# Kernel optimization log

Hardware: AMD Instinct MI355X
Metric: run time of the kernel (lower is better)

Reference implementation:

```python
import jax, jax.numpy as jnp
import numpy as np

N = 100000          # nodes
E = 1_600_000       # edges (before self loops)
F_IN = 128          # node features
H = 4               # heads (gat1)
C = 32              # dim_h
HC = H * C
NC_CLONE = 20 - 1
NC_TYPE = 30 - 1
NEG_SLOPE = 0.2
BN_EPS = 1e-5


def setup_inputs() -> dict:
    key = jax.random.key(0)
    ks = jax.random.split(key, 24)
    rn = lambda k, shape, s=0.1: (jax.random.normal(k, shape, jnp.float32) * s)
    inp = {
        "x": jax.random.normal(ks[0], (N, F_IN), jnp.float32),
        "edge_index": jax.random.randint(ks[1], (2, E), 0, N, jnp.int32),
        "edge_attr": jax.random.uniform(ks[2], (E, 1), jnp.float32),
        # gat1 (GATv2Conv F_IN -> C, heads=H, edge_dim=1)
        "Wl1": rn(ks[3], (F_IN, HC)), "Wr1": rn(ks[4], (F_IN, HC)),
        "We1": rn(ks[5], (1, HC)), "att1": rn(ks[6], (H, C)), "b1": rn(ks[7], (HC,)),
        # skip Linear F_IN -> HC
        "skip_W": rn(ks[8], (F_IN, HC)), "skip_b": rn(ks[9], (HC,)),
        # batchnorm1
        "bn_g": jnp.ones((HC,), jnp.float32), "bn_b": jnp.zeros((HC,), jnp.float32),
        # gat2 (GATv2Conv HC -> C, heads=1, edge_dim=1)
        "Wl2": rn(ks[10], (HC, C)), "Wr2": rn(ks[11], (HC, C)),
        "We2": rn(ks[12], (1, C)), "att2": rn(ks[13], (1, C)), "b2": rn(ks[14], (C,)),
        # heads
        "fc1_W": rn(ks[15], (C, C)), "fc1_b": rn(ks[16], (C,)),
        "Wc": rn(ks[17], (C, NC_CLONE)), "bc": rn(ks[18], (NC_CLONE,)),
        "Wt": rn(ks[19], (C, NC_TYPE)), "bt": rn(ks[20], (NC_TYPE,)),
    }
    return inp


def _add_self_loops(src, dst, eattr, n):
    # PyG add_self_loops with fill_value='mean': loop attr = scatter-mean of edge_attr by dst
    deg = jax.ops.segment_sum(jnp.ones_like(eattr[:, 0]), dst, num_segments=n)
    mean_attr = jax.ops.segment_sum(eattr, dst, num_segments=n) / jnp.clip(deg, 1.0)[:, None]
    loop = jnp.arange(n, dtype=src.dtype)
    return (jnp.concatenate([src, loop]), jnp.concatenate([dst, loop]),
            jnp.concatenate([eattr, mean_attr], axis=0))


def _gatv2(x, src, dst, eattr, Wl, Wr, We, att, bias, heads, ch):
    n = x.shape[0]
    xl = (x @ Wl).reshape(n, heads, ch)   # values & source attention feats
    xr = (x @ Wr).reshape(n, heads, ch)   # target attention feats
    ee = (eattr @ We).reshape(-1, heads, ch)
    m = jax.nn.leaky_relu(xl[src] + xr[dst] + ee, NEG_SLOPE)   # [E,H,C]
    alpha = jnp.einsum('ehc,hc->eh', m, att)                   # [E,H]
    amax = jax.ops.segment_max(alpha, dst, num_segments=n)
    amax = jnp.where(jnp.isfinite(amax), amax, 0.0)
    ex = jnp.exp(alpha - amax[dst])
    den = jax.ops.segment_sum(ex, dst, num_segments=n)
    a = ex / (den[dst] + 1e-16)                                # segment softmax
    out = jax.ops.segment_sum(a[..., None] * xl[src], dst, num_segments=n)
    return out.reshape(n, heads * ch) + bias, a


def reference(x, edge_index, edge_attr, Wl1, Wr1, We1, att1, b1, skip_W, skip_b,
              bn_g, bn_b, Wl2, Wr2, We2, att2, b2, fc1_W, fc1_b, Wc, bc, Wt, bt):
    n = x.shape[0]
    src, dst, ea = _add_self_loops(edge_index[0], edge_index[1], edge_attr, n)
    h, _ = _gatv2(x, src, dst, ea, Wl1, Wr1, We1, att1, b1, H, C)
    h = h + x @ skip_W + skip_b
    mu = jnp.mean(h, axis=0)
    var = jnp.mean(jnp.square(h - mu), axis=0)
    h = (h - mu) * jax.lax.rsqrt(var + BN_EPS) * bn_g + bn_b
    h = jax.nn.elu(h)
    h, w = _gatv2(h, src, dst, ea, Wl2, Wr2, We2, att2, b2, 1, C)
    h = jax.nn.elu(h)
    h_last = jax.nn.relu(h @ fc1_W + fc1_b)
    h_type = jax.nn.log_softmax(h_last @ Wt + bt, axis=1)
    h_clone = jax.nn.log_softmax(h_last @ Wc + bc, axis=1)
    out = jnp.concatenate([h_clone, h_type], axis=1)
    return out, w
```

## Files before the change

kernel.cpp:

```cpp
#include <hip/hip_runtime.h>
#include <math.h>

#define NN 100000
#define EE 1600000
#define FIN 128
#define HCH 128
#define CCH 32
#define NCLONE 19
#define NTYPE 29
#define ETOT (EE + NN)
#define SCAN_B 49

typedef __bf16 bf16_t;
typedef bf16_t bf16x2 __attribute__((ext_vector_type(2)));
typedef bf16_t bf16x4 __attribute__((ext_vector_type(4)));
typedef bf16_t bf16x8 __attribute__((ext_vector_type(8)));
typedef float f32x4 __attribute__((ext_vector_type(4)));

__global__ __launch_bounds__(256) void k_wcvt(const float* __restrict__ Wl1,
                                              const float* __restrict__ Wr1,
                                              const float* __restrict__ Ws,
                                              const float* __restrict__ Wl2,
                                              const float* __restrict__ Wr2,
                                              bf16_t* __restrict__ WbT,
                                              bf16_t* __restrict__ Wb2T) {
    int t = blockIdx.x * 256 + threadIdx.x;
    if (t < 384 * 128) {
        int n = t >> 7, k = t & 127;
        const float* W = (n < 128) ? Wl1 : ((n < 256) ? Wr1 : Ws);
        WbT[t] = (bf16_t)W[k * 128 + (n & 127)];
    } else if (t < 384 * 128 + 64 * 128) {
        int u = t - 384 * 128;
        int n = u >> 7, k = u & 127;
        const float* W = (n < 32) ? Wl2 : Wr2;
        Wb2T[u] = (bf16_t)W[k * 32 + (n & 31)];
    }
}

__global__ __launch_bounds__(256) void k_deg(const int* __restrict__ ei,
                                             int* __restrict__ deg,
                                             int* __restrict__ slot) {
    int e = blockIdx.x * 256 + threadIdx.x;
    if (e < EE) {
        int d = ei[EE + e];
        slot[e] = atomicAdd(&deg[d], 1);
    }
}

__global__ __launch_bounds__(256) void k_scan1(const int* __restrict__ deg,
                                               int* __restrict__ offs,
                                               int* __restrict__ bsum) {
    __shared__ int tsum[256];
    int b = blockIdx.x, tid = threadIdx.x;
    int base = b * 2048;
    int loc[8];
    int s = 0;
    #pragma unroll
    for (int i = 0; i < 8; ++i) {
        int idx = base + tid * 8 + i;
        int d = (idx < NN) ? deg[idx] : 0;
        loc[i] = s; s += d;
    }
    tsum[tid] = s;
    __syncthreads();
    for (int off = 1; off < 256; off <<= 1) {
        int v = (tid >= off) ? tsum[tid - off] : 0;
        __syncthreads();
        tsum[tid] += v;
        __syncthreads();
    }
    int texcl = tsum[tid] - s;
    #pragma unroll
    for (int i = 0; i < 8; ++i) {
        int idx = base + tid * 8 + i;
        if (idx < NN) offs[idx] = texcl + loc[i];
    }
    if (tid == 255) bsum[b] = tsum[255];
}

__global__ void k_scan2(int* __restrict__ bsum) {
    if (threadIdx.x == 0) {
        int run = 0;
        for (int i = 0; i < SCAN_B; ++i) { int t = bsum[i]; bsum[i] = run; run += t; }
    }
}

__global__ __launch_bounds__(256) void k_scan3(int* __restrict__ offs,
                                               const int* __restrict__ bsum) {
    int i = blockIdx.x * 256 + threadIdx.x;
    if (i < NN) offs[i] += bsum[i >> 11];
}

__global__ __launch_bounds__(256) void k_fill(const int* __restrict__ ei,
                                              const float* __restrict__ ea,
                                              const int* __restrict__ offs,
                                              const int* __restrict__ slot,
                                              int2* __restrict__ ep8,
                                              int* __restrict__ eid) {
    int e = blockIdx.x * 256 + threadIdx.x;
    if (e < EE) {
        int d = ei[EE + e];
        int pos = offs[d] + slot[e];
        ep8[pos] = make_int2(ei[e], __float_as_int(ea[e]));
        eid[pos] = e;
    }
}

__global__ __launch_bounds__(256) void k_gemm1(const float* __restrict__ x,
                                               const bf16_t* __restrict__ WbT,
                                               bf16_t* __restrict__ xl,
                                               bf16_t* __restrict__ xr,
                                               bf16_t* __restrict__ sk) {
    __shared__ bf16_t As[128 * 128];
    __shared__ bf16_t Bs[128 * 128];
    const int tid = threadIdx.x;
    const int row0 = blockIdx.x * 128;
    const int chunk = blockIdx.y;
    const int col0 = chunk * 128;
    bf16_t* __restrict__ out = (chunk == 0) ? xl : ((chunk == 1) ? xr : sk);
    #pragma unroll
    for (int i = 0; i < 8; ++i) {
        int c = i * 256 + tid;
        int r = c >> 4, g = c & 15;
        int gr = row0 + r;
        bf16x8 v = {};
        if (gr < NN) {
            float4 f0 = *(const float4*)(x + (size_t)gr * 128 + g * 8);
            float4 f1 = *(const float4*)(x + (size_t)gr * 128 + g * 8 + 4);
            v[0] = (bf16_t)f0.x; v[1] = (bf16_t)f0.y; v[2] = (bf16_t)f0.z; v[3] = (bf16_t)f0.w;
            v[4] = (bf16_t)f1.x; v[5] = (bf16_t)f1.y; v[6] = (bf16_t)f1.z; v[7] = (bf16_t)f1.w;
        }
        *(bf16x8*)&As[r * 128 + ((g ^ (r & 7)) * 8)] = v;
    }
    #pragma unroll
    for (int i = 0; i < 8; ++i) {
        int c = i * 256 + tid;
        int n = c >> 4, g = c & 15;
        bf16x8 v = *(const bf16x8*)(WbT + (size_t)(col0 + n) * 128 + g * 8);
        *(bf16x8*)&Bs[n * 128 + ((g ^ (n & 7)) * 8)] = v;
    }
    __syncthreads();

    const int wid = tid >> 6, lane = tid & 63;
    const int wm = wid >> 1, wn = wid & 1;
    const int lr = lane & 15, lg = lane >> 4;
    f32x4 acc[4][4] = {};
    #pragma unroll
    for (int ks = 0; ks < 4; ++ks) {
        int g = ks * 4 + lg;
        bf16x8 b[4];
        #pragma unroll
        for (int ni = 0; ni < 4; ++ni) {
            int n = wn * 64 + ni * 16 + lr;
            b[ni] = *(const bf16x8*)&Bs[n * 128 + ((g ^ (n & 7)) * 8)];
        }
        #pragma unroll
        for (int mi = 0; mi < 4; ++mi) {
            int r = wm * 64 + mi * 16 + lr;
            bf16x8 a = *(const bf16x8*)&As[r * 128 + ((g ^ (r & 7)) * 8)];
            #pragma unroll
            for (int ni = 0; ni < 4; ++ni)
                acc[mi][ni] = __builtin_amdgcn_mfma_f32_16x16x32_bf16(a, b[ni], acc[mi][ni], 0, 0, 0);
        }
    }
    #pragma unroll
    for (int mi = 0; mi < 4; ++mi)
        #pragma unroll
        for (int ni = 0; ni < 4; ++ni)
            #pragma unroll
            for (int j = 0; j < 4; ++j) {
                int gr = row0 + wm * 64 + mi * 16 + lg * 4 + j;
                if (gr >= NN) continue;
                int n = wn * 64 + ni * 16 + lr;
                out[(size_t)gr * 128 + n] = (bf16_t)acc[mi][ni][j];
            }
}

__global__ __launch_bounds__(256) void k_gat1(const bf16_t* __restrict__ xl1,
                                              const bf16_t* __restrict__ xr1,
                                              const bf16_t* __restrict__ skb,
                                              const int* __restrict__ offs,
                                              const int* __restrict__ deg,
                                              const int2* __restrict__ ep8,
                                              const float* __restrict__ att1,
                                              const float* __restrict__ we1,
                                              const float* __restrict__ b1,
                                              const float* __restrict__ skipb,
                                              bf16_t* __restrict__ hb,
                                              float* __restrict__ mattr) {
    int v = (blockIdx.x * 256 + threadIdx.x) >> 6;
    if (v >= NN) return;
    int lane = threadIdx.x & 63;
    int sub = lane >> 4;
    int l = lane & 15;
    int c0 = l * 8;
    float at[8], we[8], xr[8];
    {
        float4 t0 = *(const float4*)(att1 + c0);
        float4 t1 = *(const float4*)(att1 + c0 + 4);
        at[0] = t0.x; at[1] = t0.y; at[2] = t0.z; at[3] = t0.w;
        at[4] = t1.x; at[5] = t1.y; at[6] = t1.z; at[7] = t1.w;
        float4 w0 = *(const float4*)(we1 + c0);
        float4 w1 = *(const float4*)(we1 + c0 + 4);
        we[0] = w0.x; we[1] = w0.y; we[2] = w0.z; we[3] = w0.w;
        we[4] = w1.x; we[5] = w1.y; we[6] = w1.z; we[7] = w1.w;
        bf16x8 xrv = *(const bf16x8*)(xr1 + (size_t)v * 128 + c0);
        #pragma unroll
        for (int j = 0; j < 8; ++j) xr[j] = (float)xrv[j];
    }
    float mr = -1e30f, den = 0.f, easum = 0.f;
    float n[8] = {};
    int st = offs[v], dg = deg[v];
    int i = sub;
    int2 e0 = make_int2(0, 0), e1 = make_int2(0, 0);
    bf16x8 a0 = {};
    if (i < dg) e0 = ep8[st + i];
    if (i + 4 < dg) e1 = ep8[st + i + 4];
    if (i < dg) a0 = *(const bf16x8*)(xl1 + (size_t)e0.x * 128 + c0);
    for (; i < dg; i += 4) {
        bf16x8 a1 = {};
        int2 e2 = make_int2(0, 0);
        if (i + 4 < dg) a1 = *(const bf16x8*)(xl1 + (size_t)e1.x * 128 + c0);
        if (i + 8 < dg) e2 = ep8[st + i + 8];
        float ea_ = __int_as_float(e0.y);
        easum += ea_;
        float q = 0.f, xv[8];
        #pragma unroll
        for (int j = 0; j < 8; ++j) {
            xv[j] = (float)a0[j];
            float w_ = xv[j] + fmaf(ea_, we[j], xr[j]);
            w_ = (w_ > 0.f) ? w_ : 0.2f * w_;
            q = fmaf(w_, at[j], q);
        }
        q += __shfl_xor(q, 1, 4);
        q += __shfl_xor(q, 2, 4);
        float nm = fmaxf(mr, q);
        float ex = __expf(q - nm);
        if (nm > mr) {
            float sc = __expf(mr - nm);
            den *= sc;
            #pragma unroll
            for (int j = 0; j < 8; ++j) n[j] *= sc;
            mr = nm;
        }
        den += ex;
        #pragma unroll
        for (int j = 0; j < 8; ++j) n[j] = fmaf(ex, xv[j], n[j]);
        e0 = e1; a0 = a1; e1 = e2;
    }
    #pragma unroll
    for (int w_ = 16; w_ <= 32; w_ <<= 1) {
        float mo = __shfl_xor(mr, w_, 64);
        float dn = __shfl_xor(den, w_, 64);
        float es = __shfl_xor(easum, w_, 64);
        float o[8];
        #pragma unroll
        for (int j = 0; j < 8; ++j) o[j] = __shfl_xor(n[j], w_, 64);
        float M = fmaxf(mr, mo);
        float sa = __expf(mr - M), sb = __expf(mo - M);
        den = den * sa + dn * sb;
        #pragma unroll
        for (int j = 0; j < 8; ++j) n[j] = n[j] * sa + o[j] * sb;
        mr = M;
        easum += es;
    }
    float eav = easum / fmaxf((float)dg, 1.0f);
    if (lane == 0) mattr[v] = eav;
    bf16x8 svv = *(const bf16x8*)(xl1 + (size_t)v * 128 + c0);
    float qs = 0.f, xs[8];
    #pragma unroll
    for (int j = 0; j < 8; ++j) {
        xs[j] = (float)svv[j];
        float w_ = xs[j] + fmaf(eav, we[j], xr[j]);
        w_ = (w_ > 0.f) ? w_ : 0.2f * w_;
        qs = fmaf(w_, at[j], qs);
    }
    qs += __shfl_xor(qs, 1, 4);
    qs += __shfl_xor(qs, 2, 4);
    {
        float nm = fmaxf(mr, qs);
        float ex = __expf(qs - nm);
        if (nm > mr) {
            float sc = __expf(mr - nm);
            den *= sc;
            #pragma unroll
            for (int j = 0; j < 8; ++j) n[j] *= sc;
            mr = nm;
        }
        den += ex;
        #pragma unroll
        for (int j = 0; j < 8; ++j) n[j] = fmaf(ex, xs[j], n[j]);
    }
    if (sub == 0) {
        float inv = 1.0f / (den + 1e-16f);
        float4 bb0 = *(const float4*)(b1 + c0);
        float4 bb1 = *(const float4*)(b1 + c0 + 4);
        float4 sb0 = *(const float4*)(skipb + c0);
        float4 sb1 = *(const float4*)(skipb + c0 + 4);
        bf16x8 skv = *(const bf16x8*)(skb + (size_t)v * 128 + c0);
        float bb[8] = {bb0.x, bb0.y, bb0.z, bb0.w, bb1.x, bb1.y, bb1.z, bb1.w};
        float sv[8] = {sb0.x, sb0.y, sb0.z, sb0.w, sb1.x, sb1.y, sb1.z, sb1.w};
        bf16x8 r;
        #pragma unroll
        for (int j = 0; j < 8; ++j)
            r[j] = (bf16_t)(n[j] * inv + bb[j] + (float)skv[j] + sv[j]);
        *(bf16x8*)(hb + (size_t)v * 128 + c0) = r;
    }
}

__global__ __launch_bounds__(256) void k_bnstats(const bf16_t* __restrict__ h,
                                                 float* __restrict__ bns,
                                                 float* __restrict__ bnq) {
    __shared__ float sS[16 * 128];
    __shared__ float sQ[16 * 128];
    int tid = threadIdx.x;
    int cg = tid & 15;
    int slot = tid >> 4;
    int c0 = cg * 8;
    float s[8] = {}, q[8] = {};
    for (int r = blockIdx.x * 16 + slot; r < NN; r += gridDim.x * 16) {
        bf16x8 v = *(const bf16x8*)&h[(size_t)r * 128 + c0];
        #pragma unroll
        for (int j = 0; j < 8; ++j) { float f = (float)v[j]; s[j] += f; q[j] += f * f; }
    }
    #pragma unroll
    for (int j = 0; j < 8; ++j) { sS[slot * 128 + c0 + j] = s[j]; sQ[slot * 128 + c0 + j] = q[j]; }
    __syncthreads();
    if (tid < 128) {
        float as = 0.f, aq = 0.f;
        #pragma unroll
        for (int k = 0; k < 16; ++k) { as += sS[k * 128 + tid]; aq += sQ[k * 128 + tid]; }
        atomicAdd(&bns[tid], as);
        atomicAdd(&bnq[tid], aq);
    }
}

__global__ void k_bnfinal(const float* __restrict__ bns, const float* __restrict__ bnq,
                          const float* __restrict__ g, const float* __restrict__ b,
                          float* __restrict__ scale, float* __restrict__ shift) {
    int c = threadIdx.x;
    if (c < 128) {
        float mu = bns[c] * (1.0f / NN);
        float var = bnq[c] * (1.0f / NN) - mu * mu;
        float rs = rsqrtf(var + 1e-5f);
        float a = rs * g[c];
        scale[c] = a;
        shift[c] = b[c] - mu * a;
    }
}

__global__ __launch_bounds__(256) void k_gemm2(const bf16_t* __restrict__ h,
                                               const float* __restrict__ scl,
                                               const float* __restrict__ shf,
                                               const bf16_t* __restrict__ Wb2T,
                                               bf16_t* __restrict__ xl2,
                                               float* __restrict__ xr2) {
    __shared__ bf16_t As[128 * 128];
    __shared__ bf16_t Bs[64 * 128];
    const int tid = threadIdx.x;
    const int row0 = blockIdx.x * 128;
    #pragma unroll
    for (int i = 0; i < 8; ++i) {
        int c = i * 256 + tid;
        int r = c >> 4, g = c & 15;
        int gr = row0 + r;
        bf16x8 v = {};
        if (gr < NN) {
            bf16x8 hv = *(const bf16x8*)(h + (size_t)gr * 128 + g * 8);
            float4 s0 = *(const float4*)(scl + g * 8);
            float4 s1 = *(const float4*)(scl + g * 8 + 4);
            float4 t0 = *(const float4*)(shf + g * 8);
            float4 t1 = *(const float4*)(shf + g * 8 + 4);
            float e[8];
            e[0] = (float)hv[0] * s0.x + t0.x; e[1] = (float)hv[1] * s0.y + t0.y;
            e[2] = (float)hv[2] * s0.z + t0.z; e[3] = (float)hv[3] * s0.w + t0.w;
            e[4] = (float)hv[4] * s1.x + t1.x; e[5] = (float)hv[5] * s1.y + t1.y;
            e[6] = (float)hv[6] * s1.z + t1.z; e[7] = (float)hv[7] * s1.w + t1.w;
            #pragma unroll
            for (int j = 0; j < 8; ++j) {
                float vv = e[j];
                vv = (vv > 0.f) ? vv : (__expf(vv) - 1.0f);
                v[j] = (bf16_t)vv;
            }
        }
        *(bf16x8*)&As[r * 128 + ((g ^ (r & 7)) * 8)] = v;
    }
    #pragma unroll
    for (int i = 0; i < 4; ++i) {
        int c = i * 256 + tid;
        int n = c >> 4, g = c & 15;
        bf16x8 v = *(const bf16x8*)(Wb2T + (size_t)n * 128 + g * 8);
        *(bf16x8*)&Bs[n * 128 + ((g ^ (n & 7)) * 8)] = v;
    }
    __syncthreads();

    const int wid = tid >> 6, lane = tid & 63;
    const int wm = wid >> 1, wn = wid & 1;
    const int lr = lane & 15, lg = lane >> 4;
    f32x4 acc[4][2] = {};
    #pragma unroll
    for (int ks = 0; ks < 4; ++ks) {
        int g = ks * 4 + lg;
        bf16x8 b0, b1;
        {
            int n = wn * 32 + lr;
            b0 = *(const bf16x8*)&Bs[n * 128 + ((g ^ (n & 7)) * 8)];
            n += 16;
            b1 = *(const bf16x8*)&Bs[n * 128 + ((g ^ (n & 7)) * 8)];
        }
        #pragma unroll
        for (int mi = 0; mi < 4; ++mi) {
            int r = wm * 64 + mi * 16 + lr;
            bf16x8 a = *(const bf16x8*)&As[r * 128 + ((g ^ (r & 7)) * 8)];
            acc[mi][0] = __builtin_amdgcn_mfma_f32_16x16x32_bf16(a, b0, acc[mi][0], 0, 0, 0);
            acc[mi][1] = __builtin_amdgcn_mfma_f32_16x16x32_bf16(a, b1, acc[mi][1], 0, 0, 0);
        }
    }
    #pragma unroll
    for (int mi = 0; mi < 4; ++mi)
        #pragma unroll
        for (int ni = 0; ni < 2; ++ni)
            #pragma unroll
            for (int j = 0; j < 4; ++j) {
                int gr = row0 + wm * 64 + mi * 16 + lg * 4 + j;
                if (gr >= NN) continue;
                int n = wn * 32 + ni * 16 + lr;
                float val = acc[mi][ni][j];
                if (n < 32) xl2[(size_t)gr * 32 + n] = (bf16_t)val;
                else xr2[(size_t)gr * 32 + (n - 32)] = val;
            }
}

__global__ __launch_bounds__(256) void k_gat2(const bf16_t* __restrict__ xl2,
                                              const float* __restrict__ xr2,
                                              const float* __restrict__ mattr,
                                              const int* __restrict__ offs,
                                              const int* __restrict__ deg,
                                              const int2* __restrict__ ep8,
                                              const int* __restrict__ eid,
                                              const float* __restrict__ att2,
                                              const float* __restrict__ we2,
                                              const float* __restrict__ b2,
                                              float* __restrict__ h3,
                                              float* __restrict__ wout) {
    int v = (blockIdx.x * 256 + threadIdx.x) >> 6;
    if (v >= NN) return;
    int lane = threadIdx.x & 63;
    int sub = lane >> 3;
    int l = lane & 7;
    int c0 = l * 4;
    float4 atv = *(const float4*)(att2 + c0);
    float4 wev = *(const float4*)(we2 + c0);
    float4 xrv = *(const float4*)(xr2 + (size_t)v * 32 + c0);
    float at[4] = {atv.x, atv.y, atv.z, atv.w};
    float we[4] = {wev.x, wev.y, wev.z, wev.w};
    float xr[4] = {xrv.x, xrv.y, xrv.z, xrv.w};
    float mr = -1e30f, den = 0.f;
    float n[4] = {};
    int st = offs[v], dg = deg[v];
    int i = sub;
    int2 e0 = make_int2(0, 0), e1 = make_int2(0, 0);
    bf16x4 a0 = {};
    if (i < dg) e0 = ep8[st + i];
    if (i + 8 < dg) e1 = ep8[st + i + 8];
    if (i < dg) a0 = *(const bf16x4*)(xl2 + (size_t)e0.x * 32 + c0);
    for (; i < dg; i += 8) {
        bf16x4 a1 = {};
        int2 e2 = make_int2(0, 0);
        if (i + 8 < dg) a1 = *(const bf16x4*)(xl2 + (size_t)e1.x * 32 + c0);
        if (i + 16 < dg) e2 = ep8[st + i + 16];
        int ide = eid[st + i];
        float ea_ = __int_as_float(e0.y);
        float q = 0.f, xv[4];
        #pragma unroll
        for (int j = 0; j < 4; ++j) {
            xv[j] = (float)a0[j];
            float w_ = xv[j] + fmaf(ea_, we[j], xr[j]);
            w_ = (w_ > 0.f) ? w_ : 0.2f * w_;
            q = fmaf(w_, at[j], q);
        }
        q += __shfl_xor(q, 1, 8);
        q += __shfl_xor(q, 2, 8);
        q += __shfl_xor(q, 4, 8);
        if (l == 0) wout[ide] = q;
        float nm = fmaxf(mr, q);
        float ex = __expf(q - nm);
        if (nm > mr) {
            float sc = __expf(mr - nm);
            den *= sc;
            #pragma unroll
            for (int j = 0; j < 4; ++j) n[j] *= sc;
            mr = nm;
        }
        den += ex;
        #pragma unroll
        for (int j = 0; j < 4; ++j) n[j] = fmaf(ex, xv[j], n[j]);
        e0 = e1; a0 = a1; e1 = e2;
    }
    #pragma unroll
    for (int w_ = 8; w_ <= 32; w_ <<= 1) {
        float mo = __shfl_xor(mr, w_, 64);
        float dn = __shfl_xor(den, w_, 64);
        float o[4];
        #pragma unroll
        for (int j = 0; j < 4; ++j) o[j] = __shfl_xor(n[j], w_, 64);
        float M = fmaxf(mr, mo);
        float sa = __expf(mr - M), sb = __expf(mo - M);
        den = den * sa + dn * sb;
        #pragma unroll
        for (int j = 0; j < 4; ++j) n[j] = n[j] * sa + o[j] * sb;
        mr = M;
    }
    float eav = mattr[v];
    bf16x4 sv = *(const bf16x4*)(xl2 + (size_t)v * 32 + c0);
    float qs = 0.f, xs[4];
    #pragma unroll
    for (int j = 0; j < 4; ++j) {
        xs[j] = (float)sv[j];
        float w_ = xs[j] + fmaf(eav, we[j], xr[j]);
        w_ = (w_ > 0.f) ? w_ : 0.2f * w_;
        qs = fmaf(w_, at[j], qs);
    }
    qs += __shfl_xor(qs, 1, 8);
    qs += __shfl_xor(qs, 2, 8);
    qs += __shfl_xor(qs, 4, 8);
    {
        float nm = fmaxf(mr, qs);
        float ex = __expf(qs - nm);
        if (nm > mr) {
            float sc = __expf(mr - nm);
            den *= sc;
            #pragma unroll
            for (int j = 0; j < 4; ++j) n[j] *= sc;
            mr = nm;
        }
        den += ex;
        #pragma unroll
        for (int j = 0; j < 4; ++j) n[j] = fmaf(ex, xs[j], n[j]);
    }
    float inv = 1.0f / (den + 1e-16f);
    if (lane == 0) wout[EE + v] = __expf(qs - mr) * inv;
    if (l == 0) {
        for (int k = sub; k < dg; k += 8) {
            int ide = eid[st + k];
            float q = wout[ide];
            wout[ide] = __expf(q - mr) * inv;
        }
    }
    if (sub == 0) {
        float4 bb = *(const float4*)(b2 + c0);
        float b_[4] = {bb.x, bb.y, bb.z, bb.w};
        float4 r;
        float* rp = &r.x;
        #pragma unroll
        for (int j = 0; j < 4; ++j) {
            float o = n[j] * inv + b_[j];
            rp[j] = (o > 0.f) ? o : (__expf(o) - 1.0f);
        }
        *(float4*)(h3 + (size_t)v * 32 + c0) = r;
    }
}

__global__ __launch_bounds__(256) void k_head(const float* __restrict__ h3,
                                              const float* __restrict__ fc1W,
                                              const float* __restrict__ fc1b,
                                              const float* __restrict__ Wc,
                                              const float* __restrict__ bc,
                                              const float* __restrict__ Wt,
                                              const float* __restrict__ bt,
                                              float* __restrict__ outp) {
    __shared__ float sW1[32 * 32];
    __shared__ float sWc[32 * NCLONE];
    __shared__ float sWt[32 * NTYPE];
    __shared__ float sb1[32], sbc[NCLONE], sbt[NTYPE];
    int tid = threadIdx.x;
    for (int i = tid; i < 1024; i += 256) sW1[i] = fc1W[i];
    for (int i = tid; i < 32 * NCLONE; i += 256) sWc[i] = Wc[i];
    for (int i = tid; i < 32 * NTYPE; i += 256) sWt[i] = Wt[i];
    if (tid < 32) sb1[tid] = fc1b[tid];
    if (tid < NCLONE) sbc[tid] = bc[tid];
    if (tid < NTYPE) sbt[tid] = bt[tid];
    __syncthreads();
    int g = tid >> 5, l = tid & 31;
    int v = blockIdx.x * 8 + g;
    if (v >= NN) return;
    float x = h3[(size_t)v * CCH + l];
    float acc = sb1[l];
    #pragma unroll
    for (int c = 0; c < 32; ++c) {
        float xc = __shfl(x, c, 32);
        acc += xc * sW1[c * 32 + l];
    }
    float hl = fmaxf(acc, 0.0f);
    float at = (l < NTYPE) ? sbt[l] : 0.0f;
    float ac = (l < NCLONE) ? sbc[l] : 0.0f;
    #pragma unroll
    for (int c = 0; c < 32; ++c) {
        float hc = __shfl(hl, c, 32);
        float wt_ = (l < NTYPE) ? sWt[c * NTYPE + l] : 0.0f;
        float wc_ = (l < NCLONE) ? sWc[c * NCLONE + l] : 0.0f;
        at += hc * wt_;
        ac += hc * wc_;
    }
    float vt = (l < NTYPE) ? at : -INFINITY;
    float mt = vt;
    mt = fmaxf(mt, __shfl_xor(mt, 16, 32));
    mt = fmaxf(mt, __shfl_xor(mt, 8, 32));
    mt = fmaxf(mt, __shfl_xor(mt, 4, 32));
    mt = fmaxf(mt, __shfl_xor(mt, 2, 32));
    mt = fmaxf(mt, __shfl_xor(mt, 1, 32));
    float et = __expf(vt - mt);
    float stt = et;
    stt += __shfl_xor(stt, 16, 32);
    stt += __shfl_xor(stt, 8, 32);
    stt += __shfl_xor(stt, 4, 32);
    stt += __shfl_xor(stt, 2, 32);
    stt += __shfl_xor(stt, 1, 32);
    float lt = vt - mt - logf(stt);
    float vc = (l < NCLONE) ? ac : -INFINITY;
    float mc = vc;
    mc = fmaxf(mc, __shfl_xor(mc, 16, 32));
    mc = fmaxf(mc, __shfl_xor(mc, 8, 32));
    mc = fmaxf(mc, __shfl_xor(mc, 4, 32));
    mc = fmaxf(mc, __shfl_xor(mc, 2, 32));
    mc = fmaxf(mc, __shfl_xor(mc, 1, 32));
    float ec = __expf(vc - mc);
    float sc = ec;
    sc += __shfl_xor(sc, 16, 32);
    sc += __shfl_xor(sc, 8, 32);
    sc += __shfl_xor(sc, 4, 32);
    sc += __shfl_xor(sc, 2, 32);
    sc += __shfl_xor(sc, 1, 32);
    float lc = vc - mc - logf(sc);
    size_t ob = (size_t)v * 48;
    if (l < NCLONE) outp[ob + l] = lc;
    if (l < NTYPE) outp[ob + NCLONE + l] = lt;
}

extern "C" void kernel_launch(void* const* d_in, const int* in_sizes, int n_in,
                              void* d_out, int out_size, void* d_ws, size_t ws_size,
                              hipStream_t stream) {
    const float* x     = (const float*)d_in[0];
    const int*   ei    = (const int*)d_in[1];
    const float* ea    = (const float*)d_in[2];
    const float* Wl1   = (const float*)d_in[3];
    const float* Wr1   = (const float*)d_in[4];
    const float* We1   = (const float*)d_in[5];
    const float* att1  = (const float*)d_in[6];
    const float* b1    = (const float*)d_in[7];
    const float* skipW = (const float*)d_in[8];
    const float* skipb = (const float*)d_in[9];
    const float* bng   = (const float*)d_in[10];
    const float* bnb   = (const float*)d_in[11];
    const float* Wl2   = (const float*)d_in[12];
    const float* Wr2   = (const float*)d_in[13];
    const float* We2   = (const float*)d_in[14];
    const float* att2  = (const float*)d_in[15];
    const float* b2    = (const float*)d_in[16];
    const float* fc1W  = (const float*)d_in[17];
    const float* fc1b  = (const float*)d_in[18];
    const float* Wc    = (const float*)d_in[19];
    const float* bc    = (const float*)d_in[20];
    const float* Wt    = (const float*)d_in[21];
    const float* bt    = (const float*)d_in[22];
    float* out = (float*)d_out;
    float* wout = out + (size_t)NN * 48;

    const size_t NF = (size_t)NN * FIN;
    char* w = (char*)d_ws;
    bf16_t* xl1b = (bf16_t*)w;  w += NF * 2;
    bf16_t* xr1b = (bf16_t*)w;  w += NF * 2;
    bf16_t* skb  = (bf16_t*)w;  w += NF * 2;
    bf16_t* hb   = (bf16_t*)w;  w += NF * 2;
    int2*   ep8  = (int2*)w;    w += (size_t)EE * 8;
    int*    eid  = (int*)w;     w += (size_t)EE * 4;
    int*    slot = (int*)w;     w += (size_t)EE * 4;
    int* deg   = (int*)w;   w += (size_t)NN * 4;
    int* offs  = (int*)w;   w += (size_t)NN * 4;
    float* mattr = (float*)w; w += (size_t)NN * 4;
    int*   bsum  = (int*)w;   w += 64 * 4;
    float* bns   = (float*)w; w += 128 * 4;
    float* bnq   = (float*)w; w += 128 * 4;
    float* scl   = (float*)w; w += 128 * 4;
    float* shf   = (float*)w; w += 128 * 4;
    bf16_t* WbT  = (bf16_t*)w; w += 384 * 128 * 2;
    bf16_t* Wb2T = (bf16_t*)w; w += 64 * 128 * 2;
    bf16_t* xl2b = xl1b;
    float*  xr2  = (float*)xr1b;
    float*  h3   = (float*)skb;

    hipMemsetAsync(deg, 0, (size_t)NN * sizeof(int), stream);
    hipMemsetAsync(bns, 0, 256 * sizeof(float), stream);

    k_wcvt<<<224, 256, 0, stream>>>(Wl1, Wr1, skipW, Wl2, Wr2, WbT, Wb2T);

    k_deg<<<6250, 256, 0, stream>>>(ei, deg, slot);
    k_scan1<<<SCAN_B, 256, 0, stream>>>(deg, offs, bsum);
    k_scan2<<<1, 64, 0, stream>>>(bsum);
    k_scan3<<<391, 256, 0, stream>>>(offs, bsum);
    k_fill<<<6250, 256, 0, stream>>>(ei, ea, offs, slot, ep8, eid);

    k_gemm1<<<dim3(782, 3), 256, 0, stream>>>(x, WbT, xl1b, xr1b, skb);
    k_gat1<<<25000, 256, 0, stream>>>(xl1b, xr1b, skb, offs, deg, ep8,
                                      att1, We1, b1, skipb, hb, mattr);
    k_bnstats<<<128, 256, 0, stream>>>(hb, bns, bnq);
    k_bnfinal<<<1, 128, 0, stream>>>(bns, bnq, bng, bnb, scl, shf);
    k_gemm2<<<782, 256, 0, stream>>>(hb, scl, shf, Wb2T, xl2b, xr2);
    k_gat2<<<25000, 256, 0, stream>>>(xl2b, xr2, mattr, offs, deg, ep8, eid,
                                      att2, We2, b2, h3, wout);
    k_head<<<12500, 256, 0, stream>>>(h3, fc1W, fc1b, Wc, bc, Wt, bt, out);
}
```

Baseline: 485.0 us.

## Write GAT2 attention in CSR order, finalize coalesced; reuse A tile across GEMM chunks

```diff
diff --git a/kernel.cpp b/kernel.cpp
--- a/kernel.cpp
+++ b/kernel.cpp
@@ -95,14 +95,12 @@
                                               const float* __restrict__ ea,
                                               const int* __restrict__ offs,
                                               const int* __restrict__ slot,
-                                              int2* __restrict__ ep8,
-                                              int* __restrict__ eid) {
+                                              int2* __restrict__ ep8) {
     int e = blockIdx.x * 256 + threadIdx.x;
     if (e < EE) {
         int d = ei[EE + e];
         int pos = offs[d] + slot[e];
         ep8[pos] = make_int2(ei[e], __float_as_int(ea[e]));
-        eid[pos] = e;
     }
 }
 
@@ -115,9 +113,6 @@
     __shared__ bf16_t Bs[128 * 128];
     const int tid = threadIdx.x;
     const int row0 = blockIdx.x * 128;
-    const int chunk = blockIdx.y;
-    const int col0 = chunk * 128;
-    bf16_t* __restrict__ out = (chunk == 0) ? xl : ((chunk == 1) ? xr : sk);
     #pragma unroll
     for (int i = 0; i < 8; ++i) {
         int c = i * 256 + tid;
@@ -132,48 +127,55 @@
         }
         *(bf16x8*)&As[r * 128 + ((g ^ (r & 7)) * 8)] = v;
     }
-    #pragma unroll
-    for (int i = 0; i < 8; ++i) {
-        int c = i * 256 + tid;
-        int n = c >> 4, g = c & 15;
-        bf16x8 v = *(const bf16x8*)(WbT + (size_t)(col0 + n) * 128 + g * 8);
-        *(bf16x8*)&Bs[n * 128 + ((g ^ (n & 7)) * 8)] = v;
-    }
-    __syncthreads();
 
     const int wid = tid >> 6, lane = tid & 63;
     const int wm = wid >> 1, wn = wid & 1;
     const int lr = lane & 15, lg = lane >> 4;
-    f32x4 acc[4][4] = {};
-    #pragma unroll
-    for (int ks = 0; ks < 4; ++ks) {
-        int g = ks * 4 + lg;
-        bf16x8 b[4];
-        #pragma unroll
-        for (int ni = 0; ni < 4; ++ni) {
-            int n = wn * 64 + ni * 16 + lr;
-            b[ni] = *(const bf16x8*)&Bs[n * 128 + ((g ^ (n & 7)) * 8)];
-        }
-        #pragma unroll
-        for (int mi = 0; mi < 4; ++mi) {
-            int r = wm * 64 + mi * 16 + lr;
-            bf16x8 a = *(const bf16x8*)&As[r * 128 + ((g ^ (r & 7)) * 8)];
+
+    for (int chunk = 0; chunk < 3; ++chunk) {
+        const int col0 = chunk * 128;
+        bf16_t* __restrict__ out = (chunk == 0) ? xl : ((chunk == 1) ? xr : sk);
+        __syncthreads();
+        #pragma unroll
+        for (int i = 0; i < 8; ++i) {
+            int c = i * 256 + tid;
+            int n = c >> 4, g = c & 15;
+            bf16x8 v = *(const bf16x8*)(WbT + (size_t)(col0 + n) * 128 + g * 8);
+            *(bf16x8*)&Bs[n * 128 + ((g ^ (n & 7)) * 8)] = v;
+        }
+        __syncthreads();
+
+        f32x4 acc[4][4] = {};
+        #pragma unroll
+        for (int ks = 0; ks < 4; ++ks) {
+            int g = ks * 4 + lg;
+            bf16x8 b[4];
+            #pragma unroll
+            for (int ni = 0; ni < 4; ++ni) {
+                int n = wn * 64 + ni * 16 + lr;
+                b[ni] = *(const bf16x8*)&Bs[n * 128 + ((g ^ (n & 7)) * 8)];
+            }
+            #pragma unroll
+            for (int mi = 0; mi < 4; ++mi) {
+                int r = wm * 64 + mi * 16 + lr;
+                bf16x8 a = *(const bf16x8*)&As[r * 128 + ((g ^ (r & 7)) * 8)];
+                #pragma unroll
+                for (int ni = 0; ni < 4; ++ni)
+                    acc[mi][ni] = __builtin_amdgcn_mfma_f32_16x16x32_bf16(a, b[ni], acc[mi][ni], 0, 0, 0);
+            }
+        }
+        #pragma unroll
+        for (int mi = 0; mi < 4; ++mi)
             #pragma unroll
             for (int ni = 0; ni < 4; ++ni)
-                acc[mi][ni] = __builtin_amdgcn_mfma_f32_16x16x32_bf16(a, b[ni], acc[mi][ni], 0, 0, 0);
-        }
-    }
-    #pragma unroll
-    for (int mi = 0; mi < 4; ++mi)
-        #pragma unroll
-        for (int ni = 0; ni < 4; ++ni)
-            #pragma unroll
-            for (int j = 0; j < 4; ++j) {
-                int gr = row0 + wm * 64 + mi * 16 + lg * 4 + j;
-                if (gr >= NN) continue;
-                int n = wn * 64 + ni * 16 + lr;
-                out[(size_t)gr * 128 + n] = (bf16_t)acc[mi][ni][j];
-            }
+                #pragma unroll
+                for (int j = 0; j < 4; ++j) {
+                    int gr = row0 + wm * 64 + mi * 16 + lg * 4 + j;
+                    if (gr >= NN) continue;
+                    int n = wn * 64 + ni * 16 + lr;
+                    out[(size_t)gr * 128 + n] = (bf16_t)acc[mi][ni][j];
+                }
+    }
 }
 
 __global__ __launch_bounds__(256) void k_gat1(const bf16_t* __restrict__ xl1,
@@ -212,16 +214,18 @@
     float n[8] = {};
     int st = offs[v], dg = deg[v];
     int i = sub;
-    int2 e0 = make_int2(0, 0), e1 = make_int2(0, 0);
-    bf16x8 a0 = {};
+    int2 e0 = make_int2(0, 0), e1 = make_int2(0, 0), e2 = make_int2(0, 0);
+    bf16x8 a0 = {}, a1 = {};
     if (i < dg) e0 = ep8[st + i];
     if (i + 4 < dg) e1 = ep8[st + i + 4];
+    if (i + 8 < dg) e2 = ep8[st + i + 8];
     if (i < dg) a0 = *(const bf16x8*)(xl1 + (size_t)e0.x * 128 + c0);
+    if (i + 4 < dg) a1 = *(const bf16x8*)(xl1 + (size_t)e1.x * 128 + c0);
     for (; i < dg; i += 4) {
-        bf16x8 a1 = {};
-        int2 e2 = make_int2(0, 0);
-        if (i + 4 < dg) a1 = *(const bf16x8*)(xl1 + (size_t)e1.x * 128 + c0);
-        if (i + 8 < dg) e2 = ep8[st + i + 8];
+        bf16x8 a2 = {};
+        int2 e3 = make_int2(0, 0);
+        if (i + 8 < dg) a2 = *(const bf16x8*)(xl1 + (size_t)e2.x * 128 + c0);
+        if (i + 12 < dg) e3 = ep8[st + i + 12];
         float ea_ = __int_as_float(e0.y);
         easum += ea_;
         float q = 0.f, xv[8];
@@ -246,7 +250,7 @@
         den += ex;
         #pragma unroll
         for (int j = 0; j < 8; ++j) n[j] = fmaf(ex, xv[j], n[j]);
-        e0 = e1; a0 = a1; e1 = e2;
+        e0 = e1; e1 = e2; e2 = e3; a0 = a1; a1 = a2;
     }
     #pragma unroll
     for (int w_ = 16; w_ <= 32; w_ <<= 1) {
@@ -437,11 +441,12 @@
                                               const int* __restrict__ offs,
                                               const int* __restrict__ deg,
                                               const int2* __restrict__ ep8,
-                                              const int* __restrict__ eid,
                                               const float* __restrict__ att2,
                                               const float* __restrict__ we2,
                                               const float* __restrict__ b2,
                                               float* __restrict__ h3,
+                                              float* __restrict__ acsr,
+                                              float2* __restrict__ MInv,
                                               float* __restrict__ wout) {
     int v = (blockIdx.x * 256 + threadIdx.x) >> 6;
     if (v >= NN) return;
@@ -459,17 +464,18 @@
     float n[4] = {};
     int st = offs[v], dg = deg[v];
     int i = sub;
-    int2 e0 = make_int2(0, 0), e1 = make_int2(0, 0);
-    bf16x4 a0 = {};
+    int2 e0 = make_int2(0, 0), e1 = make_int2(0, 0), e2 = make_int2(0, 0);
+    bf16x4 a0 = {}, a1 = {};
     if (i < dg) e0 = ep8[st + i];
     if (i + 8 < dg) e1 = ep8[st + i + 8];
+    if (i + 16 < dg) e2 = ep8[st + i + 16];
     if (i < dg) a0 = *(const bf16x4*)(xl2 + (size_t)e0.x * 32 + c0);
+    if (i + 8 < dg) a1 = *(const bf16x4*)(xl2 + (size_t)e1.x * 32 + c0);
     for (; i < dg; i += 8) {
-        bf16x4 a1 = {};
-        int2 e2 = make_int2(0, 0);
-        if (i + 8 < dg) a1 = *(const bf16x4*)(xl2 + (size_t)e1.x * 32 + c0);
-        if (i + 16 < dg) e2 = ep8[st + i + 16];
-        int ide = eid[st + i];
+        bf16x4 a2 = {};
+        int2 e3 = make_int2(0, 0);
+        if (i + 16 < dg) a2 = *(const bf16x4*)(xl2 + (size_t)e2.x * 32 + c0);
+        if (i + 24 < dg) e3 = ep8[st + i + 24];
         float ea_ = __int_as_float(e0.y);
         float q = 0.f, xv[4];
         #pragma unroll
@@ -482,7 +488,7 @@
         q += __shfl_xor(q, 1, 8);
         q += __shfl_xor(q, 2, 8);
         q += __shfl_xor(q, 4, 8);
-        if (l == 0) wout[ide] = q;
+        if (l == 0) acsr[st + i] = q;
         float nm = fmaxf(mr, q);
         float ex = __expf(q - nm);
         if (nm > mr) {
@@ -495,7 +501,7 @@
         den += ex;
         #pragma unroll
         for (int j = 0; j < 4; ++j) n[j] = fmaf(ex, xv[j], n[j]);
-        e0 = e1; a0 = a1; e1 = e2;
+        e0 = e1; e1 = e2; e2 = e3; a0 = a1; a1 = a2;
     }
     #pragma unroll
     for (int w_ = 8; w_ <= 32; w_ <<= 1) {
@@ -539,13 +545,9 @@
         for (int j = 0; j < 4; ++j) n[j] = fmaf(ex, xs[j], n[j]);
     }
     float inv = 1.0f / (den + 1e-16f);
-    if (lane == 0) wout[EE + v] = __expf(qs - mr) * inv;
-    if (l == 0) {
-        for (int k = sub; k < dg; k += 8) {
-            int ide = eid[st + k];
-            float q = wout[ide];
-            wout[ide] = __expf(q - mr) * inv;
-        }
+    if (lane == 0) {
+        MInv[v] = make_float2(mr, inv);
+        wout[EE + v] = __expf(qs - mr) * inv;
     }
     if (sub == 0) {
         float4 bb = *(const float4*)(b2 + c0);
@@ -559,6 +561,20 @@
         }
         *(float4*)(h3 + (size_t)v * 32 + c0) = r;
     }
+}
+
+__global__ __launch_bounds__(256) void k_wfinal(const int* __restrict__ ei,
+                                                const int* __restrict__ offs,
+                                                const int* __restrict__ slot,
+                                                const float* __restrict__ acsr,
+                                                const float2* __restrict__ MInv,
+                                                float* __restrict__ wout) {
+    int e = blockIdx.x * 256 + threadIdx.x;
+    if (e >= EE) return;
+    int d = ei[EE + e];
+    float2 mi = MInv[d];
+    float al = acsr[offs[d] + slot[e]];
+    wout[e] = __expf(al - mi.x) * mi.y;
 }
 
 __global__ __launch_bounds__(256) void k_head(const float* __restrict__ h3,
@@ -673,11 +689,12 @@
     bf16_t* skb  = (bf16_t*)w;  w += NF * 2;
     bf16_t* hb   = (bf16_t*)w;  w += NF * 2;
     int2*   ep8  = (int2*)w;    w += (size_t)EE * 8;
-    int*    eid  = (int*)w;     w += (size_t)EE * 4;
+    float*  acsr = (float*)w;   w += (size_t)EE * 4;
     int*    slot = (int*)w;     w += (size_t)EE * 4;
     int* deg   = (int*)w;   w += (size_t)NN * 4;
     int* offs  = (int*)w;   w += (size_t)NN * 4;
     float* mattr = (float*)w; w += (size_t)NN * 4;
+    float2* MInv = (float2*)w; w += (size_t)NN * 8;
     int*   bsum  = (int*)w;   w += 64 * 4;
     float* bns   = (float*)w; w += 128 * 4;
     float* bnq   = (float*)w; w += 128 * 4;
@@ -698,15 +715,16 @@
     k_scan1<<<SCAN_B, 256, 0, stream>>>(deg, offs, bsum);
     k_scan2<<<1, 64, 0, stream>>>(bsum);
     k_scan3<<<391, 256, 0, stream>>>(offs, bsum);
-    k_fill<<<6250, 256, 0, stream>>>(ei, ea, offs, slot, ep8, eid);
-
-    k_gemm1<<<dim3(782, 3), 256, 0, stream>>>(x, WbT, xl1b, xr1b, skb);
+    k_fill<<<6250, 256, 0, stream>>>(ei, ea, offs, slot, ep8);
+
+    k_gemm1<<<782, 256, 0, stream>>>(x, WbT, xl1b, xr1b, skb);
     k_gat1<<<25000, 256, 0, stream>>>(xl1b, xr1b, skb, offs, deg, ep8,
                                       att1, We1, b1, skipb, hb, mattr);
     k_bnstats<<<128, 256, 0, stream>>>(hb, bns, bnq);
     k_bnfinal<<<1, 128, 0, stream>>>(bns, bnq, bng, bnb, scl, shf);
     k_gemm2<<<782, 256, 0, stream>>>(hb, scl, shf, Wb2T, xl2b, xr2);
-    k_gat2<<<25000, 256, 0, stream>>>(xl2b, xr2, mattr, offs, deg, ep8, eid,
-                                      att2, We2, b2, h3, wout);
+    k_gat2<<<25000, 256, 0, stream>>>(xl2b, xr2, mattr, offs, deg, ep8,
+                                      att2, We2, b2, h3, acsr, MInv, wout);
+    k_wfinal<<<6250, 256, 0, stream>>>(ei, offs, slot, acsr, MInv, wout);
     k_head<<<12500, 256, 0, stream>>>(h3, fc1W, fc1b, Wc, bc, Wt, bt, out);
 }
```

Result: faster. 448.8 us (-7.5%).
